# Performance work log

Hardware: AMD Instinct MI355X
Metric: run time of the kernel (lower is better)

The kernel has to match this reference:

```python
import jax, jax.numpy as jnp
import numpy as np

NUM_CLASSES = 80
INP_DIM = 608
NUM_ANCHORS = 3


def setup_inputs() -> dict:
    key = jax.random.key(0)
    B, G = 16, 76
    C = NUM_ANCHORS * (NUM_CLASSES + 5)  # 255
    prediction = jax.random.normal(key, (B, C, G, G), dtype=jnp.float32)
    anchors = jnp.array([[116.0, 90.0], [156.0, 198.0], [373.0, 326.0]], dtype=jnp.float32)
    return {"prediction": prediction, "anchors": anchors}


def reference(prediction, anchors):
    B = prediction.shape[0]
    G = prediction.shape[2]
    A = anchors.shape[0]
    NC = NUM_CLASSES
    stride = INP_DIM / G  # python float, static

    # [B, A, NC+5, G, G] -> [B, A, G, G, NC+5]
    p = prediction.reshape(B, A, NC + 5, G, G).transpose(0, 1, 3, 4, 2)

    scaled_anchors = anchors / jnp.float32(stride)          # [A, 2]
    anchor_w = scaled_anchors[:, 0].reshape(1, A, 1, 1)
    anchor_h = scaled_anchors[:, 1].reshape(1, A, 1, 1)

    x = jax.nn.sigmoid(p[..., 0])
    y = jax.nn.sigmoid(p[..., 1])
    w = p[..., 2]
    h = p[..., 3]
    pred_conf = jax.nn.sigmoid(p[..., 4])
    pred_cls = jax.nn.sigmoid(p[..., 5:])

    grid = jnp.arange(G, dtype=p.dtype)
    x_offset = grid.reshape(1, 1, 1, G)   # varies along last (column) axis
    y_offset = grid.reshape(1, 1, G, 1)   # varies along row axis

    bx = x + x_offset
    by = y + y_offset
    bw = jnp.exp(w) * anchor_w
    bh = jnp.exp(h) * anchor_h
    pred_boxes = jnp.stack([bx, by, bw, bh], axis=-1)  # [B, A, G, G, 4]

    output = jnp.concatenate(
        [
            pred_boxes.reshape(B, -1, 4) * jnp.float32(stride),
            pred_conf.reshape(B, -1, 1),
            pred_cls.reshape(B, -1, NC),
        ],
        axis=-1,
    )  # [B, A*G*G, NC+5]
    return output
```

## Files before the change

kernel.cpp:

```cpp
#include <hip/hip_runtime.h>


#define GDIM 76
#define GG 5776
#define NA 3
#define NCH 85
#define TILE 64
#define QUADS 16
#define THREADS 256
#define LOAD_UNITS (NCH * QUADS)
#define PHASE_ITERS 6

__global__ __launch_bounds__(THREADS) void yolo_kernel(
    const float* __restrict__ in, const float* __restrict__ anchors,
    float* __restrict__ out)
{
    __shared__ float lds[TILE * NCH];

    const int tile = blockIdx.x;
    const int a    = blockIdx.y;
    const int b    = blockIdx.z;
    const int s0   = tile * TILE;
    const int ba   = b * NA + a;
    const int t    = threadIdx.x;

    const float aw = anchors[a * 2 + 0];
    const float ah = anchors[a * 2 + 1];

    const float* inb = in + (long)ba * NCH * GG;

    #pragma unroll
    for (int i = 0; i < PHASE_ITERS; ++i) {
        int idx = t + i * THREADS;
        if (idx < LOAD_UNITS) {
            int c   = idx >> 4;
            int q   = idx & 15;
            int pos = s0 + q * 4;
            if (pos < GG) {
                float4 v = *reinterpret_cast<const float4*>(&inb[(long)c * GG + pos]);
                float r[4] = {v.x, v.y, v.z, v.w};
                if (c == 0) {
                    #pragma unroll
                    for (int k = 0; k < 4; ++k) {
                        int p = pos + k;
                        float gx = (float)(p - (p / GDIM) * GDIM);
                        r[k] = (1.0f / (1.0f + expf(-r[k])) + gx) * 8.0f;
                    }
                } else if (c == 1) {
                    #pragma unroll
                    for (int k = 0; k < 4; ++k) {
                        int p = pos + k;
                        float gy = (float)(p / GDIM);
                        r[k] = (1.0f / (1.0f + expf(-r[k])) + gy) * 8.0f;
                    }
                } else if (c == 2) {
                    #pragma unroll
                    for (int k = 0; k < 4; ++k) r[k] = expf(r[k]) * aw;
                } else if (c == 3) {
                    #pragma unroll
                    for (int k = 0; k < 4; ++k) r[k] = expf(r[k]) * ah;
                } else {
                    #pragma unroll
                    for (int k = 0; k < 4; ++k) r[k] = 1.0f / (1.0f + expf(-r[k]));
                }
                #pragma unroll
                for (int k = 0; k < 4; ++k)
                    lds[(q * 4 + k) * NCH + c] = r[k];
            }
        }
    }

    __syncthreads();

    const int valid  = (GG - s0 < TILE) ? (GG - s0) : TILE;
    const int nflat4 = valid * NCH / 4;
    float4* __restrict__ outv =
        reinterpret_cast<float4*>(out + ((long)ba * GG + s0) * NCH);
    const float4* ldsv = reinterpret_cast<const float4*>(lds);

    #pragma unroll
    for (int i = 0; i < PHASE_ITERS; ++i) {
        int f4 = t + i * THREADS;
        if (f4 < nflat4) {
            outv[f4] = ldsv[f4];
        }
    }
}

extern "C" void kernel_launch(void* const* d_in, const int* in_sizes, int n_in,
                              void* d_out, int out_size, void* d_ws, size_t ws_size,
                              hipStream_t stream) {
    const float* pred    = (const float*)d_in[0];
    const float* anchors = (const float*)d_in[1];
    float* out           = (float*)d_out;

    dim3 grid((GG + TILE - 1) / TILE, NA, 16);
    yolo_kernel<<<grid, THREADS, 0, stream>>>(pred, anchors, out);
}
```

Baseline: 38.12 us.

## Make kernel persistent with register prefetch of next tile over stores

Replaces the one-block-per-tile launch with a fixed grid of 1792 blocks that loop over tiles. The next tile's global loads go into registers before the current tile's LDS-to-global stores are issued, so load latency overlaps the store phase. This costs more registers, extra sync points per iteration, and fewer resident blocks than the original launch of 4368 blocks.

```diff
diff --git a/kernel.cpp b/kernel.cpp
--- a/kernel.cpp
+++ b/kernel.cpp
@@ -9,7 +9,10 @@
 #define QUADS 16
 #define THREADS 256
 #define LOAD_UNITS (NCH * QUADS)
-#define PHASE_ITERS 6
+#define LITERS 6
+#define TPB 91
+#define NT (TPB * NA * 16)
+#define GRID 1792
 
 __global__ __launch_bounds__(THREADS) void yolo_kernel(
     const float* __restrict__ in, const float* __restrict__ anchors,
@@ -17,28 +20,41 @@
 {
     __shared__ float lds[TILE * NCH];
 
-    const int tile = blockIdx.x;
-    const int a    = blockIdx.y;
-    const int b    = blockIdx.z;
-    const int s0   = tile * TILE;
-    const int ba   = b * NA + a;
-    const int t    = threadIdx.x;
+    const int t = threadIdx.x;
 
-    const float aw = anchors[a * 2 + 0];
-    const float ah = anchors[a * 2 + 1];
+    float4 v[LITERS];
 
-    const float* inb = in + (long)ba * NCH * GG;
-
-    #pragma unroll
-    for (int i = 0; i < PHASE_ITERS; ++i) {
-        int idx = t + i * THREADS;
-        if (idx < LOAD_UNITS) {
+    auto load_tile = [&](int g) {
+        int ba   = g / TPB;
+        int tile = g - ba * TPB;
+        int s0   = tile * TILE;
+        const float* inb = in + (long)ba * (NCH * GG);
+        #pragma unroll
+        for (int i = 0; i < LITERS; ++i) {
+            int idx = t + i * THREADS;
             int c   = idx >> 4;
             int q   = idx & 15;
             int pos = s0 + q * 4;
-            if (pos < GG) {
-                float4 v = *reinterpret_cast<const float4*>(&inb[(long)c * GG + pos]);
-                float r[4] = {v.x, v.y, v.z, v.w};
+            if (idx < LOAD_UNITS && pos < GG)
+                v[i] = *reinterpret_cast<const float4*>(&inb[(long)c * GG + pos]);
+        }
+    };
+
+    auto transform_write = [&](int g) {
+        int ba   = g / TPB;
+        int tile = g - ba * TPB;
+        int a    = ba % NA;
+        int s0   = tile * TILE;
+        float aw = anchors[2 * a];
+        float ah = anchors[2 * a + 1];
+        #pragma unroll
+        for (int i = 0; i < LITERS; ++i) {
+            int idx = t + i * THREADS;
+            int c   = idx >> 4;
+            int q   = idx & 15;
+            int pos = s0 + q * 4;
+            if (idx < LOAD_UNITS && pos < GG) {
+                float r[4] = {v[i].x, v[i].y, v[i].z, v[i].w};
                 if (c == 0) {
                     #pragma unroll
                     for (int k = 0; k < 4; ++k) {
@@ -68,22 +84,34 @@
                     lds[(q * 4 + k) * NCH + c] = r[k];
             }
         }
-    }
+    };
 
-    __syncthreads();
+    auto store_tile = [&](int g) {
+        int ba    = g / TPB;
+        int tile  = g - ba * TPB;
+        int s0    = tile * TILE;
+        int valid = (GG - s0 < TILE) ? (GG - s0) : TILE;
+        int n4    = valid * NCH / 4;
+        float4* __restrict__ outv =
+            reinterpret_cast<float4*>(out + ((long)ba * GG + s0) * NCH);
+        const float4* ldsv = reinterpret_cast<const float4*>(lds);
+        #pragma unroll
+        for (int i = 0; i < LITERS; ++i) {
+            int f4 = t + i * THREADS;
+            if (f4 < n4)
+                outv[f4] = ldsv[f4];
+        }
+    };
 
-    const int valid  = (GG - s0 < TILE) ? (GG - s0) : TILE;
-    const int nflat4 = valid * NCH / 4;
-    float4* __restrict__ outv =
-        reinterpret_cast<float4*>(out + ((long)ba * GG + s0) * NCH);
-    const float4* ldsv = reinterpret_cast<const float4*>(lds);
-
-    #pragma unroll
-    for (int i = 0; i < PHASE_ITERS; ++i) {
-        int f4 = t + i * THREADS;
-        if (f4 < nflat4) {
-            outv[f4] = ldsv[f4];
-        }
+    int g = blockIdx.x;
+    load_tile(g);
+    for (; g < NT; g += GRID) {
+        transform_write(g);
+        __syncthreads();
+        int gn = g + GRID;
+        if (gn < NT) load_tile(gn);
+        store_tile(g);
+        __syncthreads();
     }
 }
 
@@ -94,6 +122,5 @@
     const float* anchors = (const float*)d_in[1];
     float* out           = (float*)d_out;
 
-    dim3 grid((GG + TILE - 1) / TILE, NA, 16);
-    yolo_kernel<<<grid, THREADS, 0, stream>>>(pred, anchors, out);
+    yolo_kernel<<<dim3(GRID), dim3(THREADS), 0, stream>>>(pred, anchors, out);
 }
```

New measurement: 37.24 us. -2.3%, faster.

## Switch to persistent per-wave 16-position tiles with fast sigmoid intrinsics

Applied to the files above, without the earlier changes.

Replaces the 64-position block tiles with per-wave 16-position tiles processed in a grid-stride loop over a fixed grid. Each wave has its own LDS slice, which removes the block-wide __syncthreads. All loads for a tile are issued up front before any compute. Sigmoid and exp now use __expf and the hardware reciprocal to cut ALU cost. In exchange, each channel row is read in smaller 64-byte contiguous chunks, which may reduce memory efficiency in a kernel that is already bandwidth-bound, and the approximate math may lose some accuracy.

```diff
diff --git a/kernel.cpp b/kernel.cpp
--- a/kernel.cpp
+++ b/kernel.cpp
@@ -5,84 +5,94 @@
 #define GG 5776
 #define NA 3
 #define NCH 85
-#define TILE 64
-#define QUADS 16
+#define W 16
 #define THREADS 256
-#define LOAD_UNITS (NCH * QUADS)
-#define PHASE_ITERS 6
+#define TPW 361
+#define NTW (TPW * NA * 16)
+#define UNITS (NCH * (W / 4))
+#define WITERS 6
+#define GRID 1792
+#define NWAVES (GRID * 4)
+
+__device__ __forceinline__ float fast_sigmoid(float x) {
+    return __builtin_amdgcn_rcpf(1.0f + __expf(-x));
+}
 
 __global__ __launch_bounds__(THREADS) void yolo_kernel(
     const float* __restrict__ in, const float* __restrict__ anchors,
     float* __restrict__ out)
 {
-    __shared__ float lds[TILE * NCH];
+    __shared__ float lds[4][W * NCH];
 
-    const int tile = blockIdx.x;
-    const int a    = blockIdx.y;
-    const int b    = blockIdx.z;
-    const int s0   = tile * TILE;
-    const int ba   = b * NA + a;
-    const int t    = threadIdx.x;
+    const int wl  = threadIdx.x >> 6;
+    const int l   = threadIdx.x & 63;
+    float* slice  = &lds[wl][0];
+    const int wid = blockIdx.x * 4 + wl;
 
-    const float aw = anchors[a * 2 + 0];
-    const float ah = anchors[a * 2 + 1];
+    for (int g = wid; g < NTW; g += NWAVES) {
+        const int ba   = g / TPW;
+        const int tile = g - ba * TPW;
+        const int a    = ba % NA;
+        const int s0   = tile * W;
+        const float aw = anchors[2 * a];
+        const float ah = anchors[2 * a + 1];
+        const float* inb = in + (long)ba * (NCH * GG) + s0;
 
-    const float* inb = in + (long)ba * NCH * GG;
+        float4 v[WITERS];
 
-    #pragma unroll
-    for (int i = 0; i < PHASE_ITERS; ++i) {
-        int idx = t + i * THREADS;
-        if (idx < LOAD_UNITS) {
-            int c   = idx >> 4;
-            int q   = idx & 15;
-            int pos = s0 + q * 4;
-            if (pos < GG) {
-                float4 v = *reinterpret_cast<const float4*>(&inb[(long)c * GG + pos]);
-                float r[4] = {v.x, v.y, v.z, v.w};
+        #pragma unroll
+        for (int i = 0; i < WITERS; ++i) {
+            int u = l + i * 64;
+            if (u < UNITS) {
+                int c = u >> 2, q = u & 3;
+                v[i] = *reinterpret_cast<const float4*>(&inb[(long)c * GG + q * 4]);
+            }
+        }
+
+        #pragma unroll
+        for (int i = 0; i < WITERS; ++i) {
+            int u = l + i * 64;
+            if (u < UNITS) {
+                int c = u >> 2, q = u & 3;
+                float r[4] = {v[i].x, v[i].y, v[i].z, v[i].w};
                 if (c == 0) {
                     #pragma unroll
                     for (int k = 0; k < 4; ++k) {
-                        int p = pos + k;
+                        int p = s0 + q * 4 + k;
                         float gx = (float)(p - (p / GDIM) * GDIM);
-                        r[k] = (1.0f / (1.0f + expf(-r[k])) + gx) * 8.0f;
+                        r[k] = (fast_sigmoid(r[k]) + gx) * 8.0f;
                     }
                 } else if (c == 1) {
                     #pragma unroll
                     for (int k = 0; k < 4; ++k) {
-                        int p = pos + k;
+                        int p = s0 + q * 4 + k;
                         float gy = (float)(p / GDIM);
-                        r[k] = (1.0f / (1.0f + expf(-r[k])) + gy) * 8.0f;
+                        r[k] = (fast_sigmoid(r[k]) + gy) * 8.0f;
                     }
                 } else if (c == 2) {
                     #pragma unroll
-                    for (int k = 0; k < 4; ++k) r[k] = expf(r[k]) * aw;
+                    for (int k = 0; k < 4; ++k) r[k] = __expf(r[k]) * aw;
                 } else if (c == 3) {
                     #pragma unroll
-                    for (int k = 0; k < 4; ++k) r[k] = expf(r[k]) * ah;
+                    for (int k = 0; k < 4; ++k) r[k] = __expf(r[k]) * ah;
                 } else {
                     #pragma unroll
-                    for (int k = 0; k < 4; ++k) r[k] = 1.0f / (1.0f + expf(-r[k]));
+                    for (int k = 0; k < 4; ++k) r[k] = fast_sigmoid(r[k]);
                 }
                 #pragma unroll
                 for (int k = 0; k < 4; ++k)
-                    lds[(q * 4 + k) * NCH + c] = r[k];
+                    slice[(q * 4 + k) * NCH + c] = r[k];
             }
         }
-    }
 
-    __syncthreads();
-
-    const int valid  = (GG - s0 < TILE) ? (GG - s0) : TILE;
-    const int nflat4 = valid * NCH / 4;
-    float4* __restrict__ outv =
-        reinterpret_cast<float4*>(out + ((long)ba * GG + s0) * NCH);
-    const float4* ldsv = reinterpret_cast<const float4*>(lds);
-
-    #pragma unroll
-    for (int i = 0; i < PHASE_ITERS; ++i) {
-        int f4 = t + i * THREADS;
-        if (f4 < nflat4) {
-            outv[f4] = ldsv[f4];
+        float4* __restrict__ outv =
+            reinterpret_cast<float4*>(out + ((long)ba * GG + s0) * NCH);
+        const float4* sv = reinterpret_cast<const float4*>(slice);
+        #pragma unroll
+        for (int i = 0; i < WITERS; ++i) {
+            int f4 = l + i * 64;
+            if (f4 < UNITS)
+                outv[f4] = sv[f4];
         }
     }
 }
@@ -94,6 +104,5 @@
     const float* anchors = (const float*)d_in[1];
     float* out           = (float*)d_out;
 
-    dim3 grid((GG + TILE - 1) / TILE, NA, 16);
-    yolo_kernel<<<grid, THREADS, 0, stream>>>(pred, anchors, out);
+    yolo_kernel<<<dim3(GRID), dim3(THREADS), 0, stream>>>(pred, anchors, out);
 }
```

New measurement: 37.69 us. No clear change (-1.1%).
